# Performance work log

Measured on AMD Instinct MI355X. Metric: run time of the kernel, lower is better.

Reference implementation:

```python
import jax, jax.numpy as jnp
import numpy as np

B, N, H, DV, DSF, DEMB = 2048, 50, 128, 8, 16, 20


def setup_inputs() -> dict:
    k = jax.random.split(jax.random.key(0), 30)
    rn = lambda i, s, sc=1.0: jax.random.normal(k[i], s, dtype=jnp.float32) * sc
    w = float(1.0 / np.sqrt(H))
    return {
        "decoder_input": rn(0, (B, H)),
        "h0": rn(1, (B, H)),
        "c0": rn(2, (B, H)),
        "V_reach_mask": jax.random.bernoulli(k[3], 0.2, (B, N)),
        "start_idx": jax.random.randint(k[4], (B,), 0, N),
        "V": rn(5, (B, N, DV)),
        "start_fea": rn(6, (B, DSF)),
        "context_update": rn(7, (N, B, H)),
        "b_E": rn(8, (B, N, N)),
        "b_E_abs": rn(9, (B, N, N)),
        "H_update": rn(10, (N, B, H - 2)),
        "V_ft": rn(11, (B, N, DV)),
        "context": rn(12, (N, B, H)),
        "W_ih": rn(13, (4 * H, H), w), "W_hh": rn(14, (4 * H, H), w),
        "b_ih": rn(15, (4 * H,), w), "b_hh": rn(16, (4 * H,), w),
        "Wq_g": rn(17, (H, H), w), "bq_g": rn(18, (H,), w),
        "Wr_g": rn(19, (H, H), w), "br_g": rn(20, (H,), w),
        "v_g": rn(21, (H,), w),
        "Wq_p": rn(22, (H, H), w), "bq_p": rn(23, (H,), w),
        "Wr_p": rn(24, (H, H), w), "br_p": rn(25, (H,), w),
        "v_p": rn(26, (H,), w),
        "emb_table": rn(27, (N + 1, DEMB)),
        "W_tp": rn(28, (1, 2 * DV + DSF + DEMB), 0.1),
        "b_tp": rn(29, (1,), 0.1),
    }


def run(decoder_input, h0, c0, V_reach_mask, start_idx, V, start_fea, context_update,
        W_ih, W_hh, b_ih, b_hh, Wq_g, bq_g, Wr_g, br_g, v_g,
        Wq_p, bq_p, Wr_p, br_p, v_p, emb_table, W_tp, b_tp):
    bidx = jnp.arange(B)
    # 1x1-conv ref projections computed once: context_update is fixed across all decode steps
    e_g = jnp.einsum('od,nbd->bon', Wr_g, context_update) + br_g[None, :, None]  # [B,H,N]
    e_p = jnp.einsum('od,nbd->bon', Wr_p, context_update) + br_p[None, :, None]  # [B,H,N]

    def attn_u(q, e, v):
        # v . tanh(q + e) over feature dim -> [B,N]
        return jnp.einsum('d,bdn->bn', v, jnp.tanh(q[:, :, None] + e))

    def step(carry, t):
        h, c, mask, sel, dec_in, last_idx = carry
        # update_mask (skip scatter at t==0) + mask_modify (unmask last col if row all-True)
        scattered = mask.at[bidx, sel].set(True)
        m = jnp.where(t == 0, mask, scattered)
        m = m.at[:, -1].set(jnp.where(m.all(axis=1), False, m[:, -1]))
        # LSTMCell
        gates = dec_in @ W_ih.T + b_ih + h @ W_hh.T + b_hh
        i_, f_, g_, o_ = jnp.split(gates, 4, axis=1)
        c2 = jax.nn.sigmoid(f_) * c + jax.nn.sigmoid(i_) * jnp.tanh(g_)
        h2 = jax.nn.sigmoid(o_) * jnp.tanh(c2)
        # glimpse attention (n_glimpses = 1, mask_glimpses = True)
        q = h2 @ Wq_g.T + bq_g
        u = jnp.where(m, -jnp.inf, attn_u(q, e_g, v_g))
        a = jax.nn.softmax(u, axis=1)
        g_l = jnp.einsum('bdn,bn->bd', e_g, a)
        # pointer attention (use_tanh, C=10)
        q = g_l @ Wq_p.T + bq_p
        u = 10.0 * jnp.tanh(attn_u(q, e_p, v_p))
        u = jnp.where(m, -jnp.inf, u)
        log_p = jax.nn.log_softmax(u, axis=1)
        idxs = jnp.argmax(log_p, axis=1)
        # time prediction head (net_TP modeled as Linear(2*DV+DSF+DEMB -> 1))
        tp_in = jnp.concatenate([V[bidx, last_idx], V[bidx, idxs], start_fea,
                                 jnp.broadcast_to(emb_table[t], (B, DEMB))], axis=1)
        pred = (tp_in @ W_tp.T + b_tp)[:, 0]
        dec_next = context_update[idxs, bidx]  # rp_update_features gather
        return (h2, c2, m, idxs, dec_next, idxs), (log_p, idxs, pred)

    init = (h0, c0, V_reach_mask, jnp.zeros((B,), jnp.int32), decoder_input,
            start_idx.astype(jnp.int32))
    _, (log_p, sels, preds) = jax.lax.scan(step, init, jnp.arange(N))
    log_p = jnp.transpose(log_p, (1, 0, 2))  # [B,T,N]
    sels = sels.T                            # [B,T]
    preds = preds.T                          # [B,T]
    return log_p, sels, preds, preds[..., None]


def reference(decoder_input, h0, c0, V_reach_mask, start_idx, V, start_fea,
              context_update, b_E, b_E_abs, H_update, V_ft, context,
              W_ih, W_hh, b_ih, b_hh, Wq_g, bq_g, Wr_g, br_g, v_g,
              Wq_p, bq_p, Wr_p, br_p, v_p, emb_table, W_tp, b_tp):
    # b_E, b_E_abs, H_update, V_ft, context feed only a context tensor the original
    # loop recomputes but never reads (attention always uses context_update), so they
    # do not affect any output.
    return run(decoder_input, h0, c0, V_reach_mask, start_idx, V, start_fea,
               context_update, W_ih, W_hh, b_ih, b_hh, Wq_g, bq_g, Wr_g, br_g, v_g,
               Wq_p, bq_p, Wr_p, br_p, v_p, emb_table, W_tp, b_tp)
```

## Files before the change

kernel.cpp:

```cpp
#include <hip/hip_runtime.h>
#include <math.h>

#define BB 2048
#define NN 50
#define HH 128
#define G4 512

__device__ __forceinline__ float sigf(float x) { return 1.0f / (1.0f + expf(-x)); }

__global__ __launch_bounds__(1024) void k_prep_mask(
    const void* __restrict__ vmask_raw, unsigned char* __restrict__ mws)
{
    __shared__ int mis;
    const unsigned char* p8 = (const unsigned char*)vmask_raw;
    if (threadIdx.x == 0) mis = 0;
    __syncthreads();
    int local = 0;
    for (int i = threadIdx.x; i < BB * NN; i += 1024)
        if ((i & 3) && p8[i]) local++;
    if (local) atomicAdd(&mis, local);
    __syncthreads();
    const bool is8 = (mis != 0);
    const int* p32 = (const int*)vmask_raw;
    for (int i = threadIdx.x; i < BB * NN; i += 1024)
        mws[i] = is8 ? (p8[i] != 0) : (p32[i] != 0);
}

__global__ __launch_bounds__(256) void k_prep_transpose(
    const float* __restrict__ W_ih, const float* __restrict__ W_hh,
    const float* __restrict__ Wq_g, const float* __restrict__ Wr_g,
    const float* __restrict__ Wr_p,
    float* __restrict__ Wt_ih, float* __restrict__ Wt_hh,
    float* __restrict__ Wt_qg, float* __restrict__ Wt_rg, float* __restrict__ Wt_rp)
{
    int e = blockIdx.x * 256 + threadIdx.x;
    if (e < 65536) {
        int k = e >> 9, j = e & 511;
        Wt_ih[e] = W_ih[(size_t)j * HH + k];
        Wt_hh[e] = W_hh[(size_t)j * HH + k];
    } else {
        int e2 = e - 65536;
        if (e2 < 16384) {
            int k = e2 >> 7, o = e2 & 127;
            Wt_qg[e2] = Wq_g[(size_t)o * HH + k];
            Wt_rg[e2] = Wr_g[(size_t)o * HH + k];
            Wt_rp[e2] = Wr_p[(size_t)o * HH + k];
        }
    }
}

__global__ __launch_bounds__(128) void k_prep_mp(
    const float* __restrict__ Wq_p, const float* __restrict__ Wr_g,
    const float* __restrict__ br_g, const float* __restrict__ bq_p,
    float* __restrict__ Mt_p, float* __restrict__ c_p)
{
    int k = blockIdx.x, d = threadIdx.x;
    float acc = 0.f;
    for (int j = 0; j < HH; ++j)
        acc += Wq_p[(size_t)d * HH + j] * Wr_g[(size_t)j * HH + k];
    Mt_p[(size_t)k * HH + d] = acc;
    if (blockIdx.x == 0) {
        float cc = bq_p[d];
        for (int j = 0; j < HH; ++j) cc += Wq_p[(size_t)d * HH + j] * br_g[j];
        c_p[d] = cc;
    }
}

__global__ __launch_bounds__(256) void k_project(
    const float* __restrict__ cu,
    const float* __restrict__ Wt_rg, const float* __restrict__ Wt_rp,
    const float* __restrict__ Mt_p,
    const float* __restrict__ br_g, const float* __restrict__ br_p,
    const float* __restrict__ c_p,
    float* __restrict__ eg, float* __restrict__ ep, float* __restrict__ fp)
{
    __shared__ float xs[64][132];
    const int tid = threadIdx.x;
    const int R0 = blockIdx.x * 64;
    for (int i = 0; i < 8; ++i) {
        int f4 = i * 256 + tid;
        int r = f4 >> 5, kq = f4 & 31;
        float4 v = *reinterpret_cast<const float4*>(cu + (size_t)(R0 + r) * HH + kq * 4);
        *reinterpret_cast<float4*>(&xs[r][kq * 4]) = v;
    }
    __syncthreads();
    const int tx = tid & 31, ty = tid >> 5;
    const int c0 = tx * 4;
    const float* Wt[3] = {Wt_rg, Wt_rp, Mt_p};
    const float* bias[3] = {br_g, br_p, c_p};
    float* out[3] = {eg, ep, fp};
    for (int p = 0; p < 3; ++p) {
        const float* W = Wt[p];
        float4 bb = *reinterpret_cast<const float4*>(bias[p] + c0);
        float4 acc[8];
#pragma unroll
        for (int ii = 0; ii < 8; ++ii) acc[ii] = bb;
        for (int k = 0; k < HH; ++k) {
            float4 w = *reinterpret_cast<const float4*>(W + (size_t)k * HH + c0);
#pragma unroll
            for (int ii = 0; ii < 8; ++ii) {
                float x = xs[ty + 8 * ii][k];
                acc[ii].x += x * w.x; acc[ii].y += x * w.y;
                acc[ii].z += x * w.z; acc[ii].w += x * w.w;
            }
        }
#pragma unroll
        for (int ii = 0; ii < 8; ++ii) {
            int R = R0 + ty + 8 * ii;
            int b = R & (BB - 1), n = R >> 11;
            *reinterpret_cast<float4*>(out[p] + ((size_t)(b * NN + n)) * HH + c0) = acc[ii];
        }
    }
}

__global__ __launch_bounds__(256) void k_gates(
    int t,
    const float* __restrict__ dec0, const float* __restrict__ h0,
    const float* __restrict__ cu,
    const float* __restrict__ h_ws, const int* __restrict__ prev_idx,
    const float* __restrict__ Wt_ih, const float* __restrict__ Wt_hh,
    const float* __restrict__ b_ih, const float* __restrict__ b_hh,
    float* __restrict__ gates)
{
    __shared__ float xs[32][260];
    const int tid = threadIdx.x;
    const int b0 = (blockIdx.x >> 3) * 32, g0 = (blockIdx.x & 7) * 64;
    for (int i = 0; i < 8; ++i) {
        int f4 = i * 256 + tid;
        int bi = f4 >> 6, kq = f4 & 63;
        int k = kq * 4;
        int b = b0 + bi;
        const float* src;
        if (k < 128) {
            src = (t == 0) ? (dec0 + (size_t)b * HH + k)
                           : (cu + ((size_t)prev_idx[b] * BB + b) * HH + k);
        } else {
            src = (t == 0) ? (h0 + (size_t)b * HH + (k - 128))
                           : (h_ws + (size_t)b * HH + (k - 128));
        }
        float4 v = *reinterpret_cast<const float4*>(src);
        *reinterpret_cast<float4*>(&xs[bi][k]) = v;
    }
    __syncthreads();
    const int tx = tid & 15, ty = tid >> 4;
    const int c = g0 + tx * 4;
    float4 b1 = *reinterpret_cast<const float4*>(b_ih + c);
    float4 b2 = *reinterpret_cast<const float4*>(b_hh + c);
    float4 binit = make_float4(b1.x + b2.x, b1.y + b2.y, b1.z + b2.z, b1.w + b2.w);
    float4 acc[2];
    acc[0] = binit; acc[1] = binit;
    for (int k = 0; k < 128; ++k) {
        float4 w = *reinterpret_cast<const float4*>(Wt_ih + (size_t)k * G4 + c);
        float x0 = xs[ty][k], x1 = xs[ty + 16][k];
        acc[0].x += x0 * w.x; acc[0].y += x0 * w.y; acc[0].z += x0 * w.z; acc[0].w += x0 * w.w;
        acc[1].x += x1 * w.x; acc[1].y += x1 * w.y; acc[1].z += x1 * w.z; acc[1].w += x1 * w.w;
    }
    for (int k = 0; k < 128; ++k) {
        float4 w = *reinterpret_cast<const float4*>(Wt_hh + (size_t)k * G4 + c);
        float x0 = xs[ty][128 + k], x1 = xs[ty + 16][128 + k];
        acc[0].x += x0 * w.x; acc[0].y += x0 * w.y; acc[0].z += x0 * w.z; acc[0].w += x0 * w.w;
        acc[1].x += x1 * w.x; acc[1].y += x1 * w.y; acc[1].z += x1 * w.z; acc[1].w += x1 * w.w;
    }
    *reinterpret_cast<float4*>(gates + (size_t)(b0 + ty) * G4 + c) = acc[0];
    *reinterpret_cast<float4*>(gates + (size_t)(b0 + ty + 16) * G4 + c) = acc[1];
}

__global__ __launch_bounds__(256) void k_step(
    int t,
    const float* __restrict__ c0_in, const float* __restrict__ gates,
    float* __restrict__ c_ws, float* __restrict__ h_ws,
    const float* __restrict__ Wt_qg, const float* __restrict__ bq_g,
    const float* __restrict__ eg, const float* __restrict__ ep,
    const float* __restrict__ fp,
    const float* __restrict__ v_g, const float* __restrict__ v_p,
    const int* __restrict__ start_idx,
    const float* __restrict__ V, const float* __restrict__ sfea,
    const float* __restrict__ emb, const float* __restrict__ Wtp,
    const float* __restrict__ btp,
    unsigned char* __restrict__ mws, int* __restrict__ prev_idx,
    float* __restrict__ out_logp, float* __restrict__ out_sel,
    float* __restrict__ out_pred1, float* __restrict__ out_pred2)
{
    __shared__ float h2s[128], qs[128], vgs[128], vps[128], qps[128];
    __shared__ float part[2][128];
    __shared__ float u1[64], aa[64], u2[64];
    __shared__ unsigned char ml[64];
    const int tid = threadIdx.x;
    const int b = blockIdx.x;
    const int lane = tid & 63, wid = tid >> 6;

    if (t > 0 && tid == 128) {
        mws[b * NN + prev_idx[b]] = 1;
    }
    if (tid < 128) {
        int d = tid;
        const float* g = gates + (size_t)b * G4;
        float gi = g[d], gf = g[128 + d], gg = g[256 + d], go = g[384 + d];
        float cold = (t == 0) ? c0_in[(size_t)b * HH + d] : c_ws[(size_t)b * HH + d];
        float c2 = sigf(gf) * cold + sigf(gi) * tanhf(gg);
        float h2 = sigf(go) * tanhf(c2);
        c_ws[(size_t)b * HH + d] = c2;
        h_ws[(size_t)b * HH + d] = h2;
        h2s[d] = h2;
        vgs[d] = v_g[d];
        vps[d] = v_p[d];
    }
    __syncthreads();

    if (tid < 64) {
        int v = (tid < NN) ? (int)mws[b * NN + tid] : 1;
        unsigned long long bal = __ballot(v != 0);
        if (tid == 0 && bal == ~0ULL) mws[b * NN + (NN - 1)] = 0;
    }
    {
        int d = tid & 127, half = tid >> 7;
        float acc = 0.f;
        const float* W = Wt_qg + (size_t)(half * 64) * HH + d;
        for (int k = 0; k < 64; ++k) acc += h2s[half * 64 + k] * W[(size_t)k * HH];
        part[half][d] = acc;
    }
    __syncthreads();
    if (tid < 128) qs[tid] = part[0][tid] + part[1][tid] + bq_g[tid];
    if (tid < 64) ml[tid] = (tid < NN) ? mws[b * NN + tid] : 1;
    __syncthreads();

    for (int n = wid; n < NN; n += 4) {
        const float* er = eg + ((size_t)b * NN + n) * HH;
        float s = vgs[lane] * tanhf(qs[lane] + er[lane])
                + vgs[lane + 64] * tanhf(qs[lane + 64] + er[lane + 64]);
#pragma unroll
        for (int off = 32; off; off >>= 1) s += __shfl_xor(s, off);
        if (lane == 0) u1[n] = ml[n] ? -INFINITY : s;
    }
    __syncthreads();
    if (tid < 64) {
        float x = (tid < NN) ? u1[tid] : -INFINITY;
        float mx = x;
#pragma unroll
        for (int off = 32; off; off >>= 1) mx = fmaxf(mx, __shfl_xor(mx, off));
        float p = expf(x - mx);
        float s = p;
#pragma unroll
        for (int off = 32; off; off >>= 1) s += __shfl_xor(s, off);
        aa[tid] = p / s;
    }
    __syncthreads();
    {
        int d = tid & 127, half = tid >> 7;
        float acc = 0.f;
        const float* base = fp + (size_t)b * NN * HH + d;
        int n0 = half * 25, n1 = n0 + 25;
        for (int n = n0; n < n1; ++n) acc += aa[n] * base[(size_t)n * HH];
        part[half][d] = acc;
    }
    __syncthreads();
    if (tid < 128) qps[tid] = part[0][tid] + part[1][tid];
    __syncthreads();
    for (int n = wid; n < NN; n += 4) {
        const float* er = ep + ((size_t)b * NN + n) * HH;
        float s = vps[lane] * tanhf(qps[lane] + er[lane])
                + vps[lane + 64] * tanhf(qps[lane + 64] + er[lane + 64]);
#pragma unroll
        for (int off = 32; off; off >>= 1) s += __shfl_xor(s, off);
        if (lane == 0) u2[n] = ml[n] ? -INFINITY : 10.f * tanhf(s);
    }
    __syncthreads();
    if (tid < 64) {
        float x = (tid < NN) ? u2[tid] : -INFINITY;
        float mx = x;
#pragma unroll
        for (int off = 32; off; off >>= 1) mx = fmaxf(mx, __shfl_xor(mx, off));
        float pe = expf(x - mx);
        float s = pe;
#pragma unroll
        for (int off = 32; off; off >>= 1) s += __shfl_xor(s, off);
        float logZ = mx + logf(s);
        if (tid < NN) out_logp[((size_t)b * NN + t) * NN + tid] = fmaxf(x - logZ, -1e30f);
        unsigned long long bal = __ballot(x == mx);
        int idx = __ffsll((unsigned long long)bal) - 1;
        int last = (t == 0) ? start_idx[b] : prev_idx[b];
        float val = 0.f, w = 0.f;
        if (tid < 52) {
            w = Wtp[tid];
            if (tid < 8)       val = V[((size_t)b * NN + last) * 8 + tid];
            else if (tid < 16) val = V[((size_t)b * NN + idx) * 8 + (tid - 8)];
            else if (tid < 32) val = sfea[(size_t)b * 16 + (tid - 16)];
            else               val = emb[(size_t)t * 20 + (tid - 32)];
        }
        float pv = val * w;
#pragma unroll
        for (int off = 32; off; off >>= 1) pv += __shfl_xor(pv, off);
        if (tid == 0) {
            float pred = pv + btp[0];
            out_sel[(size_t)b * NN + t] = (float)idx;
            out_pred1[(size_t)b * NN + t] = pred;
            out_pred2[(size_t)b * NN + t] = pred;
            prev_idx[b] = idx;
        }
    }
}

extern "C" void kernel_launch(void* const* d_in, const int* in_sizes, int n_in,
                              void* d_out, int out_size, void* d_ws, size_t ws_size,
                              hipStream_t stream) {
    const float* dec0   = (const float*)d_in[0];
    const float* h0     = (const float*)d_in[1];
    const float* c0     = (const float*)d_in[2];
    const void*  vmask  = d_in[3];
    const int*   sidx   = (const int*)d_in[4];
    const float* V      = (const float*)d_in[5];
    const float* sfea   = (const float*)d_in[6];
    const float* cu     = (const float*)d_in[7];
    const float* W_ih   = (const float*)d_in[13];
    const float* W_hh   = (const float*)d_in[14];
    const float* b_ih   = (const float*)d_in[15];
    const float* b_hh   = (const float*)d_in[16];
    const float* Wq_g   = (const float*)d_in[17];
    const float* bq_g   = (const float*)d_in[18];
    const float* Wr_g   = (const float*)d_in[19];
    const float* br_g   = (const float*)d_in[20];
    const float* v_g    = (const float*)d_in[21];
    const float* Wq_p   = (const float*)d_in[22];
    const float* bq_p   = (const float*)d_in[23];
    const float* Wr_p   = (const float*)d_in[24];
    const float* br_p   = (const float*)d_in[25];
    const float* v_p    = (const float*)d_in[26];
    const float* emb    = (const float*)d_in[27];
    const float* Wtp    = (const float*)d_in[28];
    const float* btp    = (const float*)d_in[29];

    char* ws = (char*)d_ws;
    size_t off = 0;
    auto carve = [&](size_t bytes) -> void* {
        void* p = ws + off;
        off = (off + bytes + 255) & ~(size_t)255;
        return p;
    };
    float* eg     = (float*)carve((size_t)BB * NN * HH * 4);
    float* ep     = (float*)carve((size_t)BB * NN * HH * 4);
    float* fp     = (float*)carve((size_t)BB * NN * HH * 4);
    float* gates  = (float*)carve((size_t)BB * G4 * 4);
    float* h_ws   = (float*)carve((size_t)BB * HH * 4);
    float* c_ws   = (float*)carve((size_t)BB * HH * 4);
    float* Wt_ih  = (float*)carve(65536 * 4);
    float* Wt_hh  = (float*)carve(65536 * 4);
    float* Wt_qg  = (float*)carve(16384 * 4);
    float* Wt_rg  = (float*)carve(16384 * 4);
    float* Wt_rp  = (float*)carve(16384 * 4);
    float* Mt_p   = (float*)carve(16384 * 4);
    float* c_p    = (float*)carve(128 * 4);
    unsigned char* mws = (unsigned char*)carve((size_t)BB * NN);
    int* prev_idx = (int*)carve((size_t)BB * 4);

    float* out_logp  = (float*)d_out;
    float* out_sel   = out_logp + (size_t)BB * NN * NN;
    float* out_pred1 = out_sel + (size_t)BB * NN;
    float* out_pred2 = out_pred1 + (size_t)BB * NN;

    k_prep_mask<<<1, 1024, 0, stream>>>(vmask, mws);
    k_prep_transpose<<<320, 256, 0, stream>>>(W_ih, W_hh, Wq_g, Wr_g, Wr_p,
                                              Wt_ih, Wt_hh, Wt_qg, Wt_rg, Wt_rp);
    k_prep_mp<<<128, 128, 0, stream>>>(Wq_p, Wr_g, br_g, bq_p, Mt_p, c_p);
    k_project<<<(BB * NN) / 64, 256, 0, stream>>>(cu, Wt_rg, Wt_rp, Mt_p,
                                                  br_g, br_p, c_p, eg, ep, fp);
    for (int t = 0; t < NN; ++t) {
        k_gates<<<512, 256, 0, stream>>>(t, dec0, h0, cu, h_ws, prev_idx,
                                         Wt_ih, Wt_hh, b_ih, b_hh, gates);
        k_step<<<BB, 256, 0, stream>>>(t, c0, gates, c_ws, h_ws, Wt_qg, bq_g,
                                       eg, ep, fp, v_g, v_p, sidx,
                                       V, sfea, emb, Wtp, btp,
                                       mws, prev_idx, out_logp, out_sel,
                                       out_pred1, out_pred2);
    }
}
```

Measured before the change: 4.794 ms.

## Drop precomputed fp tensor, reuse eg tile in LDS and apply Wq_p per step

Removes the third B×N×H projection (fp = Wq_p·Wr_g·context) and its prep kernel. Each step now caches the eg rows in shared memory during the glimpse pass, forms the glimpse vector from that cache, and then applies Wq_p with a small per-block matvec. This cuts global memory traffic per step by one full B×N×H read and removes a 52MB workspace. It also swaps the accurate tanh, sigmoid, exp and log for fast approximations built on hardware reciprocal and __expf, and shortens the mask-type detection scan; the intrinsics change numerics slightly.

```diff
diff --git a/kernel.cpp b/kernel.cpp
--- a/kernel.cpp
+++ b/kernel.cpp
@@ -6,7 +6,13 @@
 #define HH 128
 #define G4 512
 
-__device__ __forceinline__ float sigf(float x) { return 1.0f / (1.0f + expf(-x)); }
+__device__ __forceinline__ float frcp(float x) { return __builtin_amdgcn_rcpf(x); }
+__device__ __forceinline__ float ftanh(float x) {
+    x = fminf(10.f, fmaxf(-10.f, x));
+    float e = __expf(2.f * x);
+    return (e - 1.f) * frcp(e + 1.f);
+}
+__device__ __forceinline__ float fsig(float x) { return frcp(1.f + __expf(-x)); }
 
 __global__ __launch_bounds__(1024) void k_prep_mask(
     const void* __restrict__ vmask_raw, unsigned char* __restrict__ mws)
@@ -16,7 +22,7 @@
     if (threadIdx.x == 0) mis = 0;
     __syncthreads();
     int local = 0;
-    for (int i = threadIdx.x; i < BB * NN; i += 1024)
+    for (int i = threadIdx.x; i < 16384; i += 1024)
         if ((i & 3) && p8[i]) local++;
     if (local) atomicAdd(&mis, local);
     __syncthreads();
@@ -29,9 +35,10 @@
 __global__ __launch_bounds__(256) void k_prep_transpose(
     const float* __restrict__ W_ih, const float* __restrict__ W_hh,
     const float* __restrict__ Wq_g, const float* __restrict__ Wr_g,
-    const float* __restrict__ Wr_p,
+    const float* __restrict__ Wr_p, const float* __restrict__ Wq_p,
     float* __restrict__ Wt_ih, float* __restrict__ Wt_hh,
-    float* __restrict__ Wt_qg, float* __restrict__ Wt_rg, float* __restrict__ Wt_rp)
+    float* __restrict__ Wt_qg, float* __restrict__ Wt_rg,
+    float* __restrict__ Wt_rp, float* __restrict__ Wt_qp)
 {
     int e = blockIdx.x * 256 + threadIdx.x;
     if (e < 65536) {
@@ -45,34 +52,16 @@
             Wt_qg[e2] = Wq_g[(size_t)o * HH + k];
             Wt_rg[e2] = Wr_g[(size_t)o * HH + k];
             Wt_rp[e2] = Wr_p[(size_t)o * HH + k];
-        }
-    }
-}
-
-__global__ __launch_bounds__(128) void k_prep_mp(
-    const float* __restrict__ Wq_p, const float* __restrict__ Wr_g,
-    const float* __restrict__ br_g, const float* __restrict__ bq_p,
-    float* __restrict__ Mt_p, float* __restrict__ c_p)
-{
-    int k = blockIdx.x, d = threadIdx.x;
-    float acc = 0.f;
-    for (int j = 0; j < HH; ++j)
-        acc += Wq_p[(size_t)d * HH + j] * Wr_g[(size_t)j * HH + k];
-    Mt_p[(size_t)k * HH + d] = acc;
-    if (blockIdx.x == 0) {
-        float cc = bq_p[d];
-        for (int j = 0; j < HH; ++j) cc += Wq_p[(size_t)d * HH + j] * br_g[j];
-        c_p[d] = cc;
+            Wt_qp[e2] = Wq_p[(size_t)o * HH + k];
+        }
     }
 }
 
 __global__ __launch_bounds__(256) void k_project(
     const float* __restrict__ cu,
     const float* __restrict__ Wt_rg, const float* __restrict__ Wt_rp,
-    const float* __restrict__ Mt_p,
     const float* __restrict__ br_g, const float* __restrict__ br_p,
-    const float* __restrict__ c_p,
-    float* __restrict__ eg, float* __restrict__ ep, float* __restrict__ fp)
+    float* __restrict__ eg, float* __restrict__ ep)
 {
     __shared__ float xs[64][132];
     const int tid = threadIdx.x;
@@ -86,10 +75,10 @@
     __syncthreads();
     const int tx = tid & 31, ty = tid >> 5;
     const int c0 = tx * 4;
-    const float* Wt[3] = {Wt_rg, Wt_rp, Mt_p};
-    const float* bias[3] = {br_g, br_p, c_p};
-    float* out[3] = {eg, ep, fp};
-    for (int p = 0; p < 3; ++p) {
+    const float* Wt[2] = {Wt_rg, Wt_rp};
+    const float* bias[2] = {br_g, br_p};
+    float* out[2] = {eg, ep};
+    for (int p = 0; p < 2; ++p) {
         const float* W = Wt[p];
         float4 bb = *reinterpret_cast<const float4*>(bias[p] + c0);
         float4 acc[8];
@@ -170,8 +159,8 @@
     const float* __restrict__ c0_in, const float* __restrict__ gates,
     float* __restrict__ c_ws, float* __restrict__ h_ws,
     const float* __restrict__ Wt_qg, const float* __restrict__ bq_g,
+    const float* __restrict__ Wt_qp, const float* __restrict__ bq_p,
     const float* __restrict__ eg, const float* __restrict__ ep,
-    const float* __restrict__ fp,
     const float* __restrict__ v_g, const float* __restrict__ v_p,
     const int* __restrict__ start_idx,
     const float* __restrict__ V, const float* __restrict__ sfea,
@@ -181,7 +170,8 @@
     float* __restrict__ out_logp, float* __restrict__ out_sel,
     float* __restrict__ out_pred1, float* __restrict__ out_pred2)
 {
-    __shared__ float h2s[128], qs[128], vgs[128], vps[128], qps[128];
+    __shared__ float egs[NN][HH];
+    __shared__ float h2s[128], qs[128], gls[128], qps[128];
     __shared__ float part[2][128];
     __shared__ float u1[64], aa[64], u2[64];
     __shared__ unsigned char ml[64];
@@ -189,6 +179,9 @@
     const int b = blockIdx.x;
     const int lane = tid & 63, wid = tid >> 6;
 
+    float2 vg = *reinterpret_cast<const float2*>(v_g + 2 * lane);
+    float2 vp = *reinterpret_cast<const float2*>(v_p + 2 * lane);
+
     if (t > 0 && tid == 128) {
         mws[b * NN + prev_idx[b]] = 1;
     }
@@ -197,13 +190,11 @@
         const float* g = gates + (size_t)b * G4;
         float gi = g[d], gf = g[128 + d], gg = g[256 + d], go = g[384 + d];
         float cold = (t == 0) ? c0_in[(size_t)b * HH + d] : c_ws[(size_t)b * HH + d];
-        float c2 = sigf(gf) * cold + sigf(gi) * tanhf(gg);
-        float h2 = sigf(go) * tanhf(c2);
+        float c2 = fsig(gf) * cold + fsig(gi) * ftanh(gg);
+        float h2 = fsig(go) * ftanh(c2);
         c_ws[(size_t)b * HH + d] = c2;
         h_ws[(size_t)b * HH + d] = h2;
         h2s[d] = h2;
-        vgs[d] = v_g[d];
-        vps[d] = v_p[d];
     }
     __syncthreads();
 
@@ -224,13 +215,16 @@
     if (tid < 64) ml[tid] = (tid < NN) ? mws[b * NN + tid] : 1;
     __syncthreads();
 
-    for (int n = wid; n < NN; n += 4) {
-        const float* er = eg + ((size_t)b * NN + n) * HH;
-        float s = vgs[lane] * tanhf(qs[lane] + er[lane])
-                + vgs[lane + 64] * tanhf(qs[lane + 64] + er[lane + 64]);
-#pragma unroll
-        for (int off = 32; off; off >>= 1) s += __shfl_xor(s, off);
-        if (lane == 0) u1[n] = ml[n] ? -INFINITY : s;
+    {
+        float2 qv = *reinterpret_cast<float2*>(&qs[2 * lane]);
+        for (int n = wid; n < NN; n += 4) {
+            float2 e2 = *reinterpret_cast<const float2*>(eg + ((size_t)b * NN + n) * HH + 2 * lane);
+            *reinterpret_cast<float2*>(&egs[n][2 * lane]) = e2;
+            float s = vg.x * ftanh(qv.x + e2.x) + vg.y * ftanh(qv.y + e2.y);
+#pragma unroll
+            for (int off = 32; off; off >>= 1) s += __shfl_xor(s, off);
+            if (lane == 0) u1[n] = ml[n] ? -INFINITY : s;
+        }
     }
     __syncthreads();
     if (tid < 64) {
@@ -238,7 +232,7 @@
         float mx = x;
 #pragma unroll
         for (int off = 32; off; off >>= 1) mx = fmaxf(mx, __shfl_xor(mx, off));
-        float p = expf(x - mx);
+        float p = __expf(x - mx);
         float s = p;
 #pragma unroll
         for (int off = 32; off; off >>= 1) s += __shfl_xor(s, off);
@@ -248,21 +242,32 @@
     {
         int d = tid & 127, half = tid >> 7;
         float acc = 0.f;
-        const float* base = fp + (size_t)b * NN * HH + d;
         int n0 = half * 25, n1 = n0 + 25;
-        for (int n = n0; n < n1; ++n) acc += aa[n] * base[(size_t)n * HH];
+        for (int n = n0; n < n1; ++n) acc += aa[n] * egs[n][d];
         part[half][d] = acc;
     }
     __syncthreads();
-    if (tid < 128) qps[tid] = part[0][tid] + part[1][tid];
-    __syncthreads();
-    for (int n = wid; n < NN; n += 4) {
-        const float* er = ep + ((size_t)b * NN + n) * HH;
-        float s = vps[lane] * tanhf(qps[lane] + er[lane])
-                + vps[lane + 64] * tanhf(qps[lane + 64] + er[lane + 64]);
-#pragma unroll
-        for (int off = 32; off; off >>= 1) s += __shfl_xor(s, off);
-        if (lane == 0) u2[n] = ml[n] ? -INFINITY : 10.f * tanhf(s);
+    if (tid < 128) gls[tid] = part[0][tid] + part[1][tid];
+    __syncthreads();
+    {
+        int o = tid & 127, half = tid >> 7;
+        float acc = 0.f;
+        const float* W = Wt_qp + (size_t)(half * 64) * HH + o;
+        for (int k = 0; k < 64; ++k) acc += gls[half * 64 + k] * W[(size_t)k * HH];
+        part[half][o] = acc;
+    }
+    __syncthreads();
+    if (tid < 128) qps[tid] = part[0][tid] + part[1][tid] + bq_p[tid];
+    __syncthreads();
+    {
+        float2 qv = *reinterpret_cast<float2*>(&qps[2 * lane]);
+        for (int n = wid; n < NN; n += 4) {
+            float2 e2 = *reinterpret_cast<const float2*>(ep + ((size_t)b * NN + n) * HH + 2 * lane);
+            float s = vp.x * ftanh(qv.x + e2.x) + vp.y * ftanh(qv.y + e2.y);
+#pragma unroll
+            for (int off = 32; off; off >>= 1) s += __shfl_xor(s, off);
+            if (lane == 0) u2[n] = ml[n] ? -INFINITY : 10.f * ftanh(s);
+        }
     }
     __syncthreads();
     if (tid < 64) {
@@ -270,11 +275,11 @@
         float mx = x;
 #pragma unroll
         for (int off = 32; off; off >>= 1) mx = fmaxf(mx, __shfl_xor(mx, off));
-        float pe = expf(x - mx);
+        float pe = __expf(x - mx);
         float s = pe;
 #pragma unroll
         for (int off = 32; off; off >>= 1) s += __shfl_xor(s, off);
-        float logZ = mx + logf(s);
+        float logZ = mx + __logf(s);
         if (tid < NN) out_logp[((size_t)b * NN + t) * NN + tid] = fmaxf(x - logZ, -1e30f);
         unsigned long long bal = __ballot(x == mx);
         int idx = __ffsll((unsigned long long)bal) - 1;
@@ -338,7 +343,6 @@
     };
     float* eg     = (float*)carve((size_t)BB * NN * HH * 4);
     float* ep     = (float*)carve((size_t)BB * NN * HH * 4);
-    float* fp     = (float*)carve((size_t)BB * NN * HH * 4);
     float* gates  = (float*)carve((size_t)BB * G4 * 4);
     float* h_ws   = (float*)carve((size_t)BB * HH * 4);
     float* c_ws   = (float*)carve((size_t)BB * HH * 4);
@@ -347,8 +351,7 @@
     float* Wt_qg  = (float*)carve(16384 * 4);
     float* Wt_rg  = (float*)carve(16384 * 4);
     float* Wt_rp  = (float*)carve(16384 * 4);
-    float* Mt_p   = (float*)carve(16384 * 4);
-    float* c_p    = (float*)carve(128 * 4);
+    float* Wt_qp  = (float*)carve(16384 * 4);
     unsigned char* mws = (unsigned char*)carve((size_t)BB * NN);
     int* prev_idx = (int*)carve((size_t)BB * 4);
 
@@ -358,16 +361,15 @@
     float* out_pred2 = out_pred1 + (size_t)BB * NN;
 
     k_prep_mask<<<1, 1024, 0, stream>>>(vmask, mws);
-    k_prep_transpose<<<320, 256, 0, stream>>>(W_ih, W_hh, Wq_g, Wr_g, Wr_p,
-                                              Wt_ih, Wt_hh, Wt_qg, Wt_rg, Wt_rp);
-    k_prep_mp<<<128, 128, 0, stream>>>(Wq_p, Wr_g, br_g, bq_p, Mt_p, c_p);
-    k_project<<<(BB * NN) / 64, 256, 0, stream>>>(cu, Wt_rg, Wt_rp, Mt_p,
-                                                  br_g, br_p, c_p, eg, ep, fp);
+    k_prep_transpose<<<320, 256, 0, stream>>>(W_ih, W_hh, Wq_g, Wr_g, Wr_p, Wq_p,
+                                              Wt_ih, Wt_hh, Wt_qg, Wt_rg, Wt_rp, Wt_qp);
+    k_project<<<(BB * NN) / 64, 256, 0, stream>>>(cu, Wt_rg, Wt_rp,
+                                                  br_g, br_p, eg, ep);
     for (int t = 0; t < NN; ++t) {
         k_gates<<<512, 256, 0, stream>>>(t, dec0, h0, cu, h_ws, prev_idx,
                                          Wt_ih, Wt_hh, b_ih, b_hh, gates);
         k_step<<<BB, 256, 0, stream>>>(t, c0, gates, c_ws, h_ws, Wt_qg, bq_g,
-                                       eg, ep, fp, v_g, v_p, sidx,
+                                       Wt_qp, bq_p, eg, ep, v_g, v_p, sidx,
                                        V, sfea, emb, Wtp, btp,
                                        mws, prev_idx, out_logp, out_sel,
                                        out_pred1, out_pred2);
```

New measurement: 3.871 ms. -19.3%, faster.
